# Optimization experiments

Measured on AMD Instinct MI355X. Metric: run time of the kernel, lower is better.

The kernel has to match this reference:

```python
import jax, jax.numpy as jnp
import numpy as np

B, S, D, UNITS = 8, 2048, 512, 512

def setup_inputs() -> dict:
    key = jax.random.key(0)
    k1, k2, k3, k4, k5 = jax.random.split(key, 5)
    inputs = jax.random.normal(k1, (B, S, D), dtype=jnp.float32)
    scale = 1.0 / np.sqrt(D)
    Ww = jax.random.normal(k2, (D, UNITS), dtype=jnp.float32) * scale
    Wb = jnp.zeros((UNITS,), dtype=jnp.float32)
    Uw = jax.random.normal(k3, (D, UNITS), dtype=jnp.float32) * scale
    Ub = jnp.zeros((UNITS,), dtype=jnp.float32)
    return {"inputs": inputs, "Ww": Ww, "Wb": Wb, "Uw": Uw, "Ub": Ub}

def reference(inputs, Ww, Wb, Uw, Ub):
    # query/key projections: [B,S,units]
    query = jnp.einsum('bsd,du->bsu', inputs, Ww) + Wb
    key_ = jnp.einsum('bsd,du->bsu', inputs, Uw) + Ub
    # unscaled scores [B,S,S], softmax over last axis
    scores = jnp.einsum('bqu,bku->bqk', query, key_)
    attn = jax.nn.softmax(scores, axis=-1)
    # context uses raw inputs as values
    context = jnp.einsum('bqk,bkd->bqd', attn, inputs)
    return context
```

## Files before the change

### kernel.cpp

```cpp
#include <hip/hip_runtime.h>
#include <stdint.h>

#define B_ 8
#define S_ 2048
#define D_ 512
#define U_ 512
#define M_TOTAL (B_*S_)
#define NPROJ (2*U_)
#define QBLK 64
#define KVBLK 64
#define NIT (S_/KVBLK)
#define LOG2E 1.4426950408889634f

typedef __attribute__((ext_vector_type(8))) _Float16 f16x8;
typedef __attribute__((ext_vector_type(4))) float f32x4;

__device__ __forceinline__ uint16_t f2h(float f){
  return __builtin_bit_cast(uint16_t, (_Float16)f);
}

__device__ __forceinline__ void gload16(const void* g, void* l){
  __builtin_amdgcn_global_load_lds(
      (const __attribute__((address_space(1))) void*)g,
      (__attribute__((address_space(3))) void*)l, 16, 0, 0);
}

template<int ROWS>
__device__ __forceinline__ void stage_half(char* lbase, const uint16_t* __restrict__ gpanel,
                                           int ld, int wv, int lane){
  int r0 = wv*8 + (lane>>3);
  int gs = ((lane&7) ^ (r0&7)) << 3;
  gload16(gpanel + (size_t)r0*ld + gs, lbase + wv*1024);
  if constexpr (ROWS==128){
    gload16(gpanel + (size_t)(r0+64)*ld + gs, lbase + 8192 + wv*1024);
  }
}

__global__ __launch_bounds__(256) void prep_w(const float* __restrict__ Ww,
                                              const float* __restrict__ Uw,
                                              uint16_t* __restrict__ WT){
  int idx = blockIdx.x*256 + threadIdx.x;
  int u = idx >> 9;
  int d = idx & 511;
  float v = (u < U_) ? Ww[d*U_ + u] : Uw[d*U_ + (u-U_)];
  WT[idx] = f2h(v);
}

__global__ __launch_bounds__(256) void prep_x(const float* __restrict__ X,
                                              uint16_t* __restrict__ Xf,
                                              uint16_t* __restrict__ XT){
  __shared__ float tile[32][33];
  int b = blockIdx.z;
  int s0 = blockIdx.x * 32;
  int d0 = blockIdx.y * 32;
  int tid = threadIdx.x;
  int tr = tid >> 5;
  int tc = tid & 31;
  const float* Xb = X + (size_t)b*S_*D_;
#pragma unroll
  for (int i = 0; i < 32; i += 8){
    size_t off = (size_t)(s0+tr+i)*D_ + d0+tc;
    float v = Xb[off];
    tile[tr+i][tc] = v;
    Xf[(size_t)b*S_*D_ + off] = f2h(v);
  }
  __syncthreads();
  uint16_t* XTb = XT + (size_t)b*D_*S_;
#pragma unroll
  for (int i = 0; i < 32; i += 8)
    XTb[(size_t)(d0+tr+i)*S_ + s0+tc] = f2h(tile[tc][tr+i]);
}

__global__ __launch_bounds__(512, 2) void gemm_proj(
    const uint16_t* __restrict__ A, int lda,
    const uint16_t* __restrict__ Bp, int ldb,
    uint16_t* __restrict__ Qo, uint16_t* __restrict__ Ko,
    const float* __restrict__ biasW, const float* __restrict__ biasU,
    int KD)
{
  constexpr int BMH   = 128;
  constexpr int MFR   = 8;
  constexpr int AHALF = BMH*128;
  constexpr int BHALF = 128*128;
  constexpr int DSTR  = 2*AHALF + 2*BHALF;
  __shared__ __align__(16) char smem[2*DSTR];

  const int m0 = blockIdx.y * 256;
  const int n0 = blockIdx.x * 256;
  const uint16_t* Apan = A  + (size_t)m0*lda;
  const uint16_t* Bpan = Bp + (size_t)n0*ldb;

  const int t512 = threadIdx.x;
  const int wv   = t512 >> 6;
  const int lane = t512 & 63;
  const int wm   = wv >> 2;
  const int wn   = wv & 3;
  const int fr   = lane & 15;
  const int fg   = lane >> 4;
  const int sw   = fr & 7;

  const int NT = KD >> 6;

  auto Aslot = [&](int par, int h){ return smem + par*DSTR + h*AHALF; };
  auto Bslot = [&](int par, int h){ return smem + par*DSTR + 2*AHALF + h*BHALF; };

  stage_half<128>(Aslot(0,0), Apan,                   lda, wv, lane);
  stage_half<128>(Aslot(0,1), Apan + (size_t)128*lda, lda, wv, lane);
  stage_half<128>(Bslot(0,0), Bpan,                   ldb, wv, lane);
  stage_half<128>(Bslot(0,1), Bpan + (size_t)128*ldb, ldb, wv, lane);
  if (NT > 1)
    stage_half<128>(Aslot(1,0), Apan + 64,            lda, wv, lane);
  asm volatile("s_waitcnt vmcnt(2)" ::: "memory");
  __builtin_amdgcn_s_barrier();

  f32x4 acc[MFR][4];
#pragma unroll
  for (int i=0;i<MFR;i++)
#pragma unroll
    for (int j=0;j<4;j++) acc[i][j] = (f32x4){0.f,0.f,0.f,0.f};

  for (int t = 0; t < NT; ++t){
    const int p = t & 1;
    const char* myA = Aslot(p, wm);
    const char* myB = Bslot(p, wn>>1);
    f16x8 af[MFR];

    auto rdA = [&](int ks){
#pragma unroll
      for (int mf=0; mf<MFR; ++mf)
        af[mf] = *(const f16x8*)(myA + (mf*16+fr)*128 + (((ks<<2)|fg) ^ sw)*16);
    };
    auto rdB = [&](int ks, int nh, f16x8& b0, f16x8& b1){
      int rb = (wn&1)*64 + nh*32 + fr;
      b0 = *(const f16x8*)(myB + rb*128      + (((ks<<2)|fg) ^ sw)*16);
      b1 = *(const f16x8*)(myB + (rb+16)*128 + (((ks<<2)|fg) ^ sw)*16);
    };
    auto mm = [&](int nh, f16x8 b0, f16x8 b1){
      __builtin_amdgcn_s_setprio(1);
#pragma unroll
      for (int mf=0; mf<MFR; ++mf){
        acc[mf][nh*2]   = __builtin_amdgcn_mfma_f32_16x16x32_f16(af[mf], b0, acc[mf][nh*2],   0,0,0);
        acc[mf][nh*2+1] = __builtin_amdgcn_mfma_f32_16x16x32_f16(af[mf], b1, acc[mf][nh*2+1], 0,0,0);
      }
      __builtin_amdgcn_s_setprio(0);
    };

    f16x8 b0, b1;
    rdA(0); rdB(0, 0, b0, b1);
    if (t+1 < NT)
      stage_half<128>(Aslot(p^1,1), Apan + (size_t)128*lda + (t+1)*64, lda, wv, lane);
    __builtin_amdgcn_s_barrier();
    mm(0, b0, b1);
    __builtin_amdgcn_s_barrier();
    rdB(0, 1, b0, b1);
    if (t+1 < NT)
      stage_half<128>(Bslot(p^1,0), Bpan + (t+1)*64, ldb, wv, lane);
    __builtin_amdgcn_s_barrier();
    mm(1, b0, b1);
    __builtin_amdgcn_s_barrier();
    rdA(1); rdB(1, 0, b0, b1);
    if (t+1 < NT)
      stage_half<128>(Bslot(p^1,1), Bpan + (size_t)128*ldb + (t+1)*64, ldb, wv, lane);
    __builtin_amdgcn_s_barrier();
    mm(0, b0, b1);
    __builtin_amdgcn_s_barrier();
    rdB(1, 1, b0, b1);
    if (t+2 < NT)
      stage_half<128>(Aslot(p,0), Apan + (t+2)*64, lda, wv, lane);
    __builtin_amdgcn_s_barrier();
    mm(1, b0, b1);
    asm volatile("s_waitcnt vmcnt(2)" ::: "memory");
    __builtin_amdgcn_s_barrier();
  }

#pragma unroll
  for (int mf=0; mf<MFR; ++mf)
#pragma unroll
    for (int nf=0; nf<4; ++nf){
      int col  = n0 + wn*64 + nf*16 + fr;
      int rowb = m0 + wm*128 + mf*16 + fg*4;
      f32x4 a = acc[mf][nf];
      float bias = (col < U_) ? biasW[col] : biasU[col - U_];
      if (col < U_){
#pragma unroll
        for (int r=0;r<4;r++) Qo[(size_t)(rowb+r)*U_ + col] = f2h((a[r] + bias)*LOG2E);
      } else {
#pragma unroll
        for (int r=0;r<4;r++) Ko[(size_t)(rowb+r)*U_ + col - U_] = f2h(a[r] + bias);
      }
    }
}

__global__ __launch_bounds__(512, 2) void flash_attn(
    const uint16_t* __restrict__ Qf,
    const uint16_t* __restrict__ Kf,
    const uint16_t* __restrict__ XT,
    float* __restrict__ Out)
{
  __shared__ __align__(16) uint16_t Ks[KVBLK][512];
  __shared__ __align__(16) float    Ss[2][QBLK][68];
  __shared__ __align__(16) uint16_t Ps[QBLK][KVBLK];
  __shared__ float m_s[QBLK], l_s[QBLK], f_s[QBLK];

  const int bid   = blockIdx.x;
  const int batch = bid & 7;
  const int s0    = (bid >> 3) * QBLK;

  const int t    = threadIdx.x;
  const int wv   = t >> 6;
  const int lane = t & 63;
  const int fr   = lane & 15;
  const int fg   = lane >> 4;
  const int qh   = wv >> 2;
  const int kh   = (wv >> 1) & 1;
  const int ks_  = wv & 1;
  const int wd   = wv;
  const int srow = wv*8 + (lane & 7);
  const int sj   = lane >> 3;

  const uint16_t* Krow = Kf + (size_t)batch*S_*U_;
  const uint16_t* Vt   = XT + (size_t)batch*D_*S_;

  f16x8 qreg[2][8];
  {
    const uint16_t* Qbase = Qf + ((size_t)batch*S_ + s0 + qh*32)*U_ + ks_*256;
#pragma unroll
    for (int ti=0; ti<2; ++ti)
#pragma unroll
      for (int kk=0; kk<8; ++kk)
        qreg[ti][kk] = *(const f16x8*)(Qbase + (size_t)(ti*16+fr)*U_ + kk*32 + fg*8);
  }

  auto stageK = [&](int ti){
    const uint16_t* src = Krow + (size_t)(ti*KVBLK)*U_;
#pragma unroll
    for (int i=0;i<8;++i){
      int r = i*8 + wv;
      gload16(src + (size_t)r*U_ + ((lane ^ (r&7))<<3),
              (char*)Ks + i*8192 + wv*1024);
    }
  };

  stageK(0);
  if (t < QBLK){ m_s[t] = -3e38f; l_s[t] = 0.f; }
  f32x4 acc[4][4];
#pragma unroll
  for (int i=0;i<4;i++)
#pragma unroll
    for (int j=0;j<4;j++) acc[i][j] = (f32x4){0.f,0.f,0.f,0.f};
  asm volatile("s_waitcnt vmcnt(0) lgkmcnt(0)" ::: "memory");
  __builtin_amdgcn_s_barrier();
  __builtin_amdgcn_sched_barrier(0);

  for (int it=0; it<NIT; ++it){
    f32x4 sfr[2][2];
#pragma unroll
    for (int a=0;a<2;a++)
#pragma unroll
      for (int b=0;b<2;b++) sfr[a][b] = (f32x4){0.f,0.f,0.f,0.f};
    {
      const int krow0 = kh*32 + fr;
      const int krow1 = kh*32 + 16 + fr;
      const char* Kb0 = (const char*)Ks + krow0*1024;
      const char* Kb1 = (const char*)Ks + krow1*1024;
      const int swz0 = krow0 & 7, swz1 = krow1 & 7;
      __builtin_amdgcn_s_setprio(1);
#pragma unroll
      for (int kk=0; kk<8; ++kk){
        int g = (ks_<<5) | (kk<<2) | fg;
        f16x8 b0 = *(const f16x8*)(Kb0 + ((g ^ swz0)<<4));
        f16x8 b1 = *(const f16x8*)(Kb1 + ((g ^ swz1)<<4));
        sfr[0][0] = __builtin_amdgcn_mfma_f32_16x16x32_f16(qreg[0][kk], b0, sfr[0][0], 0,0,0);
        sfr[0][1] = __builtin_amdgcn_mfma_f32_16x16x32_f16(qreg[0][kk], b1, sfr[0][1], 0,0,0);
        sfr[1][0] = __builtin_amdgcn_mfma_f32_16x16x32_f16(qreg[1][kk], b0, sfr[1][0], 0,0,0);
        sfr[1][1] = __builtin_amdgcn_mfma_f32_16x16x32_f16(qreg[1][kk], b1, sfr[1][1], 0,0,0);
      }
      __builtin_amdgcn_s_setprio(0);
    }
#pragma unroll
    for (int ti=0; ti<2; ++ti)
#pragma unroll
      for (int kvf=0; kvf<2; ++kvf)
#pragma unroll
        for (int r=0; r<4; ++r)
          Ss[ks_][qh*32 + ti*16 + fg*4 + r][kh*32 + kvf*16 + fr] = sfr[ti][kvf][r];
    asm volatile("s_waitcnt lgkmcnt(0)" ::: "memory");
    __builtin_amdgcn_s_barrier();
    __builtin_amdgcn_sched_barrier(0);

    f16x8 vreg[2][4];
#pragma unroll
    for (int vk=0; vk<2; ++vk)
#pragma unroll
      for (int dt=0; dt<4; ++dt)
        vreg[vk][dt] = *(const f16x8*)(Vt + (size_t)(wd*64 + dt*16 + fr)*S_
                                       + it*KVBLK + vk*32 + fg*8);
    stageK((it+1) & (NIT-1));
    __builtin_amdgcn_sched_barrier(0);

    {
      float4 a0 = *(const float4*)&Ss[0][srow][sj*8];
      float4 a1 = *(const float4*)&Ss[0][srow][sj*8+4];
      float4 c0 = *(const float4*)&Ss[1][srow][sj*8];
      float4 c1 = *(const float4*)&Ss[1][srow][sj*8+4];
      float v0 = a0.x+c0.x, v1 = a0.y+c0.y, v2 = a0.z+c0.z, v3 = a0.w+c0.w;
      float v4 = a1.x+c1.x, v5 = a1.y+c1.y, v6 = a1.z+c1.z, v7 = a1.w+c1.w;
      float pm = fmaxf(fmaxf(fmaxf(v0,v1),fmaxf(v2,v3)),
                       fmaxf(fmaxf(v4,v5),fmaxf(v6,v7)));
      pm = fmaxf(pm, __shfl_xor(pm, 8));
      pm = fmaxf(pm, __shfl_xor(pm, 16));
      pm = fmaxf(pm, __shfl_xor(pm, 32));
      float mo = m_s[srow];
      float mn = (pm > mo + 11.54f) ? pm : mo;
      float p0 = __builtin_amdgcn_exp2f(v0-mn), p1 = __builtin_amdgcn_exp2f(v1-mn);
      float p2 = __builtin_amdgcn_exp2f(v2-mn), p3 = __builtin_amdgcn_exp2f(v3-mn);
      float p4 = __builtin_amdgcn_exp2f(v4-mn), p5 = __builtin_amdgcn_exp2f(v5-mn);
      float p6 = __builtin_amdgcn_exp2f(v6-mn), p7 = __builtin_amdgcn_exp2f(v7-mn);
      float sum = ((p0+p1)+(p2+p3)) + ((p4+p5)+(p6+p7));
      sum += __shfl_xor(sum, 8);
      sum += __shfl_xor(sum, 16);
      sum += __shfl_xor(sum, 32);
      if (sj == 0){
        float f = __builtin_amdgcn_exp2f(mo - mn);
        f_s[srow] = f;
        m_s[srow] = mn;
        l_s[srow] = l_s[srow]*f + sum;
      }
      uint32_t w0 = (uint32_t)f2h(p0) | ((uint32_t)f2h(p1)<<16);
      uint32_t w1 = (uint32_t)f2h(p2) | ((uint32_t)f2h(p3)<<16);
      uint32_t w2 = (uint32_t)f2h(p4) | ((uint32_t)f2h(p5)<<16);
      uint32_t w3 = (uint32_t)f2h(p6) | ((uint32_t)f2h(p7)<<16);
      uint4 pw = make_uint4(w0,w1,w2,w3);
      *(uint4*)((char*)Ps + srow*128 + ((sj ^ (srow&7))<<4)) = pw;
    }
    asm volatile("s_waitcnt lgkmcnt(0)" ::: "memory");
    __builtin_amdgcn_s_barrier();
    __builtin_amdgcn_sched_barrier(0);

    {
      float fx[4][4];
#pragma unroll
      for (int qt=0; qt<4; ++qt)
#pragma unroll
        for (int r=0; r<4; ++r)
          fx[qt][r] = f_s[qt*16 + fg*4 + r];
      bool nr = false;
#pragma unroll
      for (int qt=0; qt<4; ++qt)
#pragma unroll
        for (int r=0; r<4; ++r) nr = nr | (fx[qt][r] != 1.f);
      if (__any(nr)){
#pragma unroll
        for (int qt=0; qt<4; ++qt)
#pragma unroll
          for (int dt=0; dt<4; ++dt)
#pragma unroll
            for (int r=0; r<4; ++r)
              acc[qt][dt][r] *= fx[qt][r];
      }
    }

    __builtin_amdgcn_s_setprio(1);
#pragma unroll
    for (int vk=0; vk<2; ++vk){
      f16x8 pa[4];
#pragma unroll
      for (int qt=0; qt<4; ++qt){
        int q = qt*16 + fr;
        pa[qt] = *(const f16x8*)((const char*)Ps + q*128 + ((((vk<<2)|fg) ^ (q&7))<<4));
      }
#pragma unroll
      for (int qt=0; qt<4; ++qt)
#pragma unroll
        for (int dt=0; dt<4; ++dt)
          acc[qt][dt] = __builtin_amdgcn_mfma_f32_16x16x32_f16(pa[qt], vreg[vk][dt], acc[qt][dt], 0,0,0);
    }
    __builtin_amdgcn_s_setprio(0);
    asm volatile("s_waitcnt vmcnt(0)" ::: "memory");
    __builtin_amdgcn_s_barrier();
    __builtin_amdgcn_sched_barrier(0);
  }

  float linv[4][4];
#pragma unroll
  for (int qt=0; qt<4; ++qt)
#pragma unroll
    for (int r=0; r<4; ++r)
      linv[qt][r] = 1.0f / l_s[qt*16 + fg*4 + r];
  float* Ob = Out + ((size_t)batch*S_ + s0)*D_;
#pragma unroll
  for (int qt=0; qt<4; ++qt)
#pragma unroll
    for (int dt=0; dt<4; ++dt){
      int d = wd*64 + dt*16 + fr;
#pragma unroll
      for (int r=0; r<4; ++r){
        int q = qt*16 + fg*4 + r;
        Ob[(size_t)q*D_ + d] = acc[qt][dt][r] * linv[qt][r];
      }
    }
}

extern "C" void kernel_launch(void* const* d_in, const int* in_sizes, int n_in,
                              void* d_out, int out_size, void* d_ws, size_t ws_size,
                              hipStream_t stream)
{
  (void)in_sizes; (void)n_in; (void)out_size; (void)ws_size;
  const float* X  = (const float*)d_in[0];
  const float* Ww = (const float*)d_in[1];
  const float* Wb = (const float*)d_in[2];
  const float* Uw = (const float*)d_in[3];
  const float* Ub = (const float*)d_in[4];
  float* out = (float*)d_out;

  char* ws = (char*)d_ws;
  size_t off = 0;
  uint16_t* Xf = (uint16_t*)(ws + off); off += (size_t)M_TOTAL*D_*2;
  uint16_t* XT = (uint16_t*)(ws + off); off += (size_t)B_*D_*S_*2;
  uint16_t* WT = (uint16_t*)(ws + off); off += (size_t)NPROJ*D_*2;
  uint16_t* Qf = (uint16_t*)(ws + off); off += (size_t)M_TOTAL*U_*2;
  uint16_t* Kf = (uint16_t*)(ws + off); off += (size_t)M_TOTAL*U_*2;

  prep_w<<<dim3((NPROJ*D_)/256), 256, 0, stream>>>(Ww, Uw, WT);
  prep_x<<<dim3(S_/32, D_/32, B_), 256, 0, stream>>>(X, Xf, XT);

  gemm_proj<<<dim3(NPROJ/256, M_TOTAL/256, 1), 512, 0, stream>>>(
      Xf, D_, WT, D_, Qf, Kf, Wb, Ub, D_);

  flash_attn<<<dim3(B_ * (S_/QBLK)), 512, 0, stream>>>(Qf, Kf, XT, out);
}
```

Measured before the change: 182.1 us.

## Shrink attention query tile to 32 rows, keep Q in LDS and stream K from global

The flash attention kernel now handles 32 queries per block with 4 waves instead of 64 with 8. Q is staged once into LDS, and each wave loads K fragments straight from global memory into registers every iteration, so the shared K staging buffer is gone. Each wave covers 128 output columns, and the trailing per-iteration barrier is removed. This doubles the grid and cuts LDS use, which should raise occupancy. The cost is that K and V are read from global twice as often overall, and K global-load latency is no longer hidden by prefetching.

```diff
diff --git a/kernel.cpp b/kernel.cpp
--- a/kernel.cpp
+++ b/kernel.cpp
@@ -7,7 +7,7 @@
 #define U_ 512
 #define M_TOTAL (B_*S_)
 #define NPROJ (2*U_)
-#define QBLK 64
+#define QBLK 32
 #define KVBLK 64
 #define NIT (S_/KVBLK)
 #define LOG2E 1.4426950408889634f
@@ -191,13 +191,13 @@
     }
 }
 
-__global__ __launch_bounds__(512, 2) void flash_attn(
+__global__ __launch_bounds__(256, 2) void flash_attn(
     const uint16_t* __restrict__ Qf,
     const uint16_t* __restrict__ Kf,
     const uint16_t* __restrict__ XT,
     float* __restrict__ Out)
 {
-  __shared__ __align__(16) uint16_t Ks[KVBLK][512];
+  __shared__ __align__(16) uint16_t Qs[QBLK][512];
   __shared__ __align__(16) float    Ss[2][QBLK][68];
   __shared__ __align__(16) uint16_t Ps[QBLK][KVBLK];
   __shared__ float m_s[QBLK], l_s[QBLK], f_s[QBLK];
@@ -211,91 +211,79 @@
   const int lane = t & 63;
   const int fr   = lane & 15;
   const int fg   = lane >> 4;
-  const int qh   = wv >> 2;
-  const int kh   = (wv >> 1) & 1;
-  const int ks_  = wv & 1;
+  const int kh   = wv & 1;
+  const int ks_  = wv >> 1;
   const int wd   = wv;
-  const int srow = wv*8 + (lane & 7);
-  const int sj   = lane >> 3;
+  const int srow = t >> 3;
+  const int sj   = t & 7;
 
   const uint16_t* Krow = Kf + (size_t)batch*S_*U_;
   const uint16_t* Vt   = XT + (size_t)batch*D_*S_;
 
-  f16x8 qreg[2][8];
   {
-    const uint16_t* Qbase = Qf + ((size_t)batch*S_ + s0 + qh*32)*U_ + ks_*256;
-#pragma unroll
-    for (int ti=0; ti<2; ++ti)
-#pragma unroll
-      for (int kk=0; kk<8; ++kk)
-        qreg[ti][kk] = *(const f16x8*)(Qbase + (size_t)(ti*16+fr)*U_ + kk*32 + fg*8);
+    const uint16_t* Qb = Qf + ((size_t)batch*S_ + s0)*U_;
+#pragma unroll
+    for (int i=0;i<8;++i){
+      int row = i*4 + wv;
+      gload16(Qb + (size_t)row*U_ + ((lane ^ (row&7))<<3),
+              (char*)Qs + i*4096 + wv*1024);
+    }
   }
-
-  auto stageK = [&](int ti){
-    const uint16_t* src = Krow + (size_t)(ti*KVBLK)*U_;
-#pragma unroll
-    for (int i=0;i<8;++i){
-      int r = i*8 + wv;
-      gload16(src + (size_t)r*U_ + ((lane ^ (r&7))<<3),
-              (char*)Ks + i*8192 + wv*1024);
-    }
-  };
-
-  stageK(0);
   if (t < QBLK){ m_s[t] = -3e38f; l_s[t] = 0.f; }
-  f32x4 acc[4][4];
-#pragma unroll
-  for (int i=0;i<4;i++)
-#pragma unroll
-    for (int j=0;j<4;j++) acc[i][j] = (f32x4){0.f,0.f,0.f,0.f};
+  f32x4 acc[2][8];
+#pragma unroll
+  for (int i=0;i<2;i++)
+#pragma unroll
+    for (int j=0;j<8;j++) acc[i][j] = (f32x4){0.f,0.f,0.f,0.f};
   asm volatile("s_waitcnt vmcnt(0) lgkmcnt(0)" ::: "memory");
   __builtin_amdgcn_s_barrier();
   __builtin_amdgcn_sched_barrier(0);
 
   for (int it=0; it<NIT; ++it){
+    f16x8 kreg[2][8];
+    {
+      const uint16_t* Kb = Krow + (size_t)(it*KVBLK + kh*32)*U_ + ks_*256;
+#pragma unroll
+      for (int kvf=0; kvf<2; ++kvf)
+#pragma unroll
+        for (int kk=0; kk<8; ++kk)
+          kreg[kvf][kk] = *(const f16x8*)(Kb + (size_t)(kvf*16+fr)*U_ + kk*32 + fg*8);
+    }
     f32x4 sfr[2][2];
 #pragma unroll
     for (int a=0;a<2;a++)
 #pragma unroll
       for (int b=0;b<2;b++) sfr[a][b] = (f32x4){0.f,0.f,0.f,0.f};
-    {
-      const int krow0 = kh*32 + fr;
-      const int krow1 = kh*32 + 16 + fr;
-      const char* Kb0 = (const char*)Ks + krow0*1024;
-      const char* Kb1 = (const char*)Ks + krow1*1024;
-      const int swz0 = krow0 & 7, swz1 = krow1 & 7;
-      __builtin_amdgcn_s_setprio(1);
-#pragma unroll
-      for (int kk=0; kk<8; ++kk){
-        int g = (ks_<<5) | (kk<<2) | fg;
-        f16x8 b0 = *(const f16x8*)(Kb0 + ((g ^ swz0)<<4));
-        f16x8 b1 = *(const f16x8*)(Kb1 + ((g ^ swz1)<<4));
-        sfr[0][0] = __builtin_amdgcn_mfma_f32_16x16x32_f16(qreg[0][kk], b0, sfr[0][0], 0,0,0);
-        sfr[0][1] = __builtin_amdgcn_mfma_f32_16x16x32_f16(qreg[0][kk], b1, sfr[0][1], 0,0,0);
-        sfr[1][0] = __builtin_amdgcn_mfma_f32_16x16x32_f16(qreg[1][kk], b0, sfr[1][0], 0,0,0);
-        sfr[1][1] = __builtin_amdgcn_mfma_f32_16x16x32_f16(qreg[1][kk], b1, sfr[1][1], 0,0,0);
-      }
-      __builtin_amdgcn_s_setprio(0);
-    }
-#pragma unroll
-    for (int ti=0; ti<2; ++ti)
+    __builtin_amdgcn_s_setprio(1);
+#pragma unroll
+    for (int kk=0; kk<8; ++kk){
+      int g = (ks_<<5) | (kk<<2) | fg;
+      f16x8 aq0 = *(const f16x8*)((const char*)Qs + (fr)*1024      + ((g ^ (fr&7))<<4));
+      f16x8 aq1 = *(const f16x8*)((const char*)Qs + (16+fr)*1024   + ((g ^ (fr&7))<<4));
+      sfr[0][0] = __builtin_amdgcn_mfma_f32_16x16x32_f16(aq0, kreg[0][kk], sfr[0][0], 0,0,0);
+      sfr[0][1] = __builtin_amdgcn_mfma_f32_16x16x32_f16(aq0, kreg[1][kk], sfr[0][1], 0,0,0);
+      sfr[1][0] = __builtin_amdgcn_mfma_f32_16x16x32_f16(aq1, kreg[0][kk], sfr[1][0], 0,0,0);
+      sfr[1][1] = __builtin_amdgcn_mfma_f32_16x16x32_f16(aq1, kreg[1][kk], sfr[1][1], 0,0,0);
+    }
+    __builtin_amdgcn_s_setprio(0);
+#pragma unroll
+    for (int qt=0; qt<2; ++qt)
 #pragma unroll
       for (int kvf=0; kvf<2; ++kvf)
 #pragma unroll
         for (int r=0; r<4; ++r)
-          Ss[ks_][qh*32 + ti*16 + fg*4 + r][kh*32 + kvf*16 + fr] = sfr[ti][kvf][r];
+          Ss[ks_][qt*16 + fg*4 + r][kh*32 + kvf*16 + fr] = sfr[qt][kvf][r];
     asm volatile("s_waitcnt lgkmcnt(0)" ::: "memory");
     __builtin_amdgcn_s_barrier();
     __builtin_amdgcn_sched_barrier(0);
 
-    f16x8 vreg[2][4];
+    f16x8 vreg[2][8];
 #pragma unroll
     for (int vk=0; vk<2; ++vk)
 #pragma unroll
-      for (int dt=0; dt<4; ++dt)
-        vreg[vk][dt] = *(const f16x8*)(Vt + (size_t)(wd*64 + dt*16 + fr)*S_
+      for (int dt=0; dt<8; ++dt)
+        vreg[vk][dt] = *(const f16x8*)(Vt + (size_t)(wd*128 + dt*16 + fr)*S_
                                        + it*KVBLK + vk*32 + fg*8);
-    stageK((it+1) & (NIT-1));
     __builtin_amdgcn_sched_barrier(0);
 
     {
@@ -307,9 +295,9 @@
       float v4 = a1.x+c1.x, v5 = a1.y+c1.y, v6 = a1.z+c1.z, v7 = a1.w+c1.w;
       float pm = fmaxf(fmaxf(fmaxf(v0,v1),fmaxf(v2,v3)),
                        fmaxf(fmaxf(v4,v5),fmaxf(v6,v7)));
-      pm = fmaxf(pm, __shfl_xor(pm, 8));
-      pm = fmaxf(pm, __shfl_xor(pm, 16));
-      pm = fmaxf(pm, __shfl_xor(pm, 32));
+      pm = fmaxf(pm, __shfl_xor(pm, 1));
+      pm = fmaxf(pm, __shfl_xor(pm, 2));
+      pm = fmaxf(pm, __shfl_xor(pm, 4));
       float mo = m_s[srow];
       float mn = (pm > mo + 11.54f) ? pm : mo;
       float p0 = __builtin_amdgcn_exp2f(v0-mn), p1 = __builtin_amdgcn_exp2f(v1-mn);
@@ -317,9 +305,9 @@
       float p4 = __builtin_amdgcn_exp2f(v4-mn), p5 = __builtin_amdgcn_exp2f(v5-mn);
       float p6 = __builtin_amdgcn_exp2f(v6-mn), p7 = __builtin_amdgcn_exp2f(v7-mn);
       float sum = ((p0+p1)+(p2+p3)) + ((p4+p5)+(p6+p7));
-      sum += __shfl_xor(sum, 8);
-      sum += __shfl_xor(sum, 16);
-      sum += __shfl_xor(sum, 32);
+      sum += __shfl_xor(sum, 1);
+      sum += __shfl_xor(sum, 2);
+      sum += __shfl_xor(sum, 4);
       if (sj == 0){
         float f = __builtin_amdgcn_exp2f(mo - mn);
         f_s[srow] = f;
@@ -338,22 +326,19 @@
     __builtin_amdgcn_sched_barrier(0);
 
     {
-      float fx[4][4];
-#pragma unroll
-      for (int qt=0; qt<4; ++qt)
+      float fx[2][4];
+#pragma unroll
+      for (int qt=0; qt<2; ++qt)
 #pragma unroll
         for (int r=0; r<4; ++r)
           fx[qt][r] = f_s[qt*16 + fg*4 + r];
-      bool nr = false;
-#pragma unroll
-      for (int qt=0; qt<4; ++qt)
-#pragma unroll
-        for (int r=0; r<4; ++r) nr = nr | (fx[qt][r] != 1.f);
+      bool nr = (fx[0][0]!=1.f)|(fx[0][1]!=1.f)|(fx[0][2]!=1.f)|(fx[0][3]!=1.f)|
+                (fx[1][0]!=1.f)|(fx[1][1]!=1.f)|(fx[1][2]!=1.f)|(fx[1][3]!=1.f);
       if (__any(nr)){
 #pragma unroll
-        for (int qt=0; qt<4; ++qt)
-#pragma unroll
-          for (int dt=0; dt<4; ++dt)
+        for (int qt=0; qt<2; ++qt)
+#pragma unroll
+          for (int dt=0; dt<8; ++dt)
 #pragma unroll
             for (int r=0; r<4; ++r)
               acc[qt][dt][r] *= fx[qt][r];
@@ -363,36 +348,33 @@
     __builtin_amdgcn_s_setprio(1);
 #pragma unroll
     for (int vk=0; vk<2; ++vk){
-      f16x8 pa[4];
-#pragma unroll
-      for (int qt=0; qt<4; ++qt){
+      f16x8 pa[2];
+#pragma unroll
+      for (int qt=0; qt<2; ++qt){
         int q = qt*16 + fr;
         pa[qt] = *(const f16x8*)((const char*)Ps + q*128 + ((((vk<<2)|fg) ^ (q&7))<<4));
       }
 #pragma unroll
-      for (int qt=0; qt<4; ++qt)
-#pragma unroll
-        for (int dt=0; dt<4; ++dt)
+      for (int qt=0; qt<2; ++qt)
+#pragma unroll
+        for (int dt=0; dt<8; ++dt)
           acc[qt][dt] = __builtin_amdgcn_mfma_f32_16x16x32_f16(pa[qt], vreg[vk][dt], acc[qt][dt], 0,0,0);
     }
     __builtin_amdgcn_s_setprio(0);
-    asm volatile("s_waitcnt vmcnt(0)" ::: "memory");
-    __builtin_amdgcn_s_barrier();
-    __builtin_amdgcn_sched_barrier(0);
   }
 
-  float linv[4][4];
-#pragma unroll
-  for (int qt=0; qt<4; ++qt)
+  float linv[2][4];
+#pragma unroll
+  for (int qt=0; qt<2; ++qt)
 #pragma unroll
     for (int r=0; r<4; ++r)
       linv[qt][r] = 1.0f / l_s[qt*16 + fg*4 + r];
   float* Ob = Out + ((size_t)batch*S_ + s0)*D_;
 #pragma unroll
-  for (int qt=0; qt<4; ++qt)
-#pragma unroll
-    for (int dt=0; dt<4; ++dt){
-      int d = wd*64 + dt*16 + fr;
+  for (int qt=0; qt<2; ++qt)
+#pragma unroll
+    for (int dt=0; dt<8; ++dt){
+      int d = wd*128 + dt*16 + fr;
 #pragma unroll
       for (int r=0; r<4; ++r){
         int q = qt*16 + fg*4 + r;
@@ -427,5 +409,5 @@
   gemm_proj<<<dim3(NPROJ/256, M_TOTAL/256, 1), 512, 0, stream>>>(
       Xf, D_, WT, D_, Qf, Kf, Wb, Ub, D_);
 
-  flash_attn<<<dim3(B_ * (S_/QBLK)), 512, 0, stream>>>(Qf, Kf, XT, out);
-}
+  flash_attn<<<dim3(B_ * (S_/QBLK)), 256, 0, stream>>>(Qf, Kf, XT, out);
+}
```

After: 287.6 us. +57.9%, slower.
